# Optimization experiments

Hardware: AMD Instinct MI355X
Metric: run time of the kernel (lower is better)

Reference implementation:

```python
import jax, jax.numpy as jnp
import numpy as np

EPS = 1e-7
NC = 80
REG_MAX = 16
TOPK = 10
ALPHA = 0.5
BETA = 6.0
BOX_GAIN = 7.5
CLS_GAIN = 0.5
DFL_GAIN = 1.5
GRID = 92  # GRID*GRID = 8464 anchors


def _make_anchors(n):
    c = jnp.arange(n, dtype=jnp.float32) + 0.5
    gy, gx = jnp.meshgrid(c, c, indexing='ij')
    return jnp.stack([gx.ravel(), gy.ravel()], axis=-1)  # (n*n, 2)


def setup_inputs() -> dict:
    key = jax.random.key(0)
    ks = jax.random.split(key, 8)
    B, M, A = 32, 64, GRID * GRID
    anchor_points = _make_anchors(GRID)
    pred_scores = jax.random.normal(ks[0], (B, A, NC), jnp.float32)
    pred_dist = jax.random.normal(ks[1], (B, A, 4 * REG_MAX), jnp.float32)
    # decoded pred boxes: anchor center +- positive ltrb offsets (grid units)
    off = jax.random.uniform(ks[2], (B, A, 4), jnp.float32, 0.5, 12.0)
    ap = anchor_points[None]
    pred_bboxes = jnp.concatenate([ap - off[..., :2], ap + off[..., 2:]], axis=-1)
    cxy = jax.random.uniform(ks[3], (B, M, 2), jnp.float32, 4.0, 88.0)
    wh = jax.random.uniform(ks[4], (B, M, 2), jnp.float32, 2.0, 24.0)
    gt_bboxes = jnp.concatenate([cxy - wh / 2, cxy + wh / 2], axis=-1)
    gt_labels = jax.random.randint(ks[5], (B, M, 1), 0, NC, jnp.int32)
    mask_gt = (jax.random.uniform(ks[6], (B, M, 1)) < 0.75).astype(jnp.float32)
    return dict(pred_scores=pred_scores, pred_dist=pred_dist, pred_bboxes=pred_bboxes,
                anchor_points=anchor_points, gt_labels=gt_labels, gt_bboxes=gt_bboxes,
                mask_gt=mask_gt)


def _assign(pred_scores, pred_bboxes, anchor_points, gt_labels, gt_bboxes, mask_gt):
    """TaskAlignedAssigner (runs under stop_gradient at call site)."""
    B, A, nc = pred_scores.shape
    M = gt_labels.shape[1]
    scores = jax.nn.sigmoid(pred_scores)  # (B,A,nc)
    gt = gt_bboxes[:, :, None, :]         # (B,M,1,4)
    pd = pred_bboxes[:, None, :, :]       # (B,1,A,4)
    iw = jnp.clip(jnp.minimum(gt[..., 2], pd[..., 2]) - jnp.maximum(gt[..., 0], pd[..., 0]), 0)
    ih = jnp.clip(jnp.minimum(gt[..., 3], pd[..., 3]) - jnp.maximum(gt[..., 1], pd[..., 1]), 0)
    inter = iw * ih
    a_gt = (gt[..., 2] - gt[..., 0]) * (gt[..., 3] - gt[..., 1])
    a_pd = (pd[..., 2] - pd[..., 0]) * (pd[..., 3] - pd[..., 1])
    overlaps = inter / (a_gt + a_pd - inter + EPS)  # (B,M,A)
    cls = jnp.clip(gt_labels[..., 0].astype(jnp.int32), 0, nc - 1)  # (B,M)
    idx = jnp.broadcast_to(cls[:, :, None], (B, M, A))
    align_scores = jnp.take_along_axis(scores.transpose(0, 2, 1), idx, axis=1)  # (B,M,A)
    align_metric = (align_scores ** ALPHA) * (overlaps ** BETA) * mask_gt
    k = min(TOPK, A)
    _, topk_idxs = jax.lax.top_k(align_metric, k)  # (B,M,k)
    cmask = jnp.zeros((B, M, A), bool).at[
        jnp.arange(B)[:, None, None], jnp.arange(M)[None, :, None], topk_idxs].set(True)
    # anchor center strictly inside GT box
    ax = anchor_points[None, None, :, 0]
    ay = anchor_points[None, None, :, 1]
    d = jnp.stack([ax - gt_bboxes[:, :, None, 0], ay - gt_bboxes[:, :, None, 1],
                   gt_bboxes[:, :, None, 2] - ax, gt_bboxes[:, :, None, 3] - ay], axis=-1)
    in_gt = d.min(axis=-1) > EPS  # (B,M,A)
    cmask = cmask & (mask_gt > 0) & in_gt
    fg_mask = cmask.any(axis=1)  # (B,A)
    mm = align_metric * cmask
    tgi = jnp.argmax(mm, axis=1)  # (B,A)
    tlab = jnp.take_along_axis(cls, tgi, axis=1) * fg_mask.astype(jnp.int32)
    tbox = jnp.take_along_axis(gt_bboxes, tgi[:, :, None], axis=1)  # (B,A,4)
    max_per_gt = mm.max(axis=2)  # (B,M)
    am = jnp.take_along_axis(align_metric, tgi[:, None, :], axis=1)[:, 0, :]  # (B,A)
    den = jnp.take_along_axis(max_per_gt, tgi, axis=1) + EPS
    norm_score = jnp.where(fg_mask, am / den, 0.0)
    tscores = jax.nn.one_hot(tlab, nc, dtype=pred_scores.dtype) * norm_score[..., None] * fg_mask[..., None]
    return tlab, tbox, tscores, fg_mask, tgi


def _ciou(b1, b2):
    """Element-wise CIoU for aligned box pairs, xyxy, (..., 4) -> (...)."""
    x11, y11, x21, y21 = (b1[..., i] for i in range(4))
    x12, y12, x22, y22 = (b2[..., i] for i in range(4))
    iw = jnp.clip(jnp.minimum(x21, x22) - jnp.maximum(x11, x12), 0)
    ih = jnp.clip(jnp.minimum(y21, y22) - jnp.maximum(y11, y12), 0)
    inter = iw * ih
    a1 = (x21 - x11) * (y21 - y11)
    a2 = (x22 - x12) * (y22 - y12)
    iou = inter / (a1 + a2 - inter + EPS)
    cw = jnp.maximum(x21, x22) - jnp.minimum(x11, x12)
    ch = jnp.maximum(y21, y22) - jnp.minimum(y11, y12)
    c2 = cw ** 2 + ch ** 2 + EPS
    rho2 = ((x11 + x21 - x12 - x22) ** 2 + (y11 + y21 - y12 - y22) ** 2) / 4
    w1, h1 = x21 - x11, y21 - y11
    w2, h2 = x22 - x12, y22 - y12
    v = (4.0 / jnp.pi ** 2) * (jnp.arctan(w1 / (h1 + EPS)) - jnp.arctan(w2 / (h2 + EPS))) ** 2
    alpha = jax.lax.stop_gradient(v / (1 - iou + v + EPS))
    return iou - (rho2 / c2 + v * alpha)


def _loss(pred_scores, pred_dist, pred_bboxes, anchor_points, gt_labels, gt_bboxes, mask_gt):
    asg = _assign(pred_scores, pred_bboxes, anchor_points, gt_labels, gt_bboxes, mask_gt)
    tlab, tbox, tscores, fg_mask, tgi = jax.tree_util.tree_map(jax.lax.stop_gradient, asg)
    fgf = fg_mask.astype(pred_scores.dtype)
    tss = jnp.maximum(tscores.sum(), 1.0)
    # classification: BCE with logits, summed, normalized by target_scores_sum
    x = pred_scores
    bce = jnp.maximum(x, 0) - x * tscores + jnp.log1p(jnp.exp(-jnp.abs(x)))
    loss_cls = bce.sum() / tss
    # CIoU loss over foreground anchors (masked, static shapes)
    weight = tscores.sum(-1) * fgf  # (B,A)
    iou = _ciou(pred_bboxes, tbox)
    loss_iou = ((1.0 - iou) * weight).sum() / tss
    # DFL: bbox2dist targets clipped to [0, reg_max-1-0.01]
    ap = anchor_points[None]
    t = jnp.concatenate([ap - tbox[..., :2], tbox[..., 2:] - ap], axis=-1)  # (B,A,4)
    t = jnp.clip(t, 0.0, REG_MAX - 1 - 0.01)
    tl = t.astype(jnp.int32)
    tr = jnp.minimum(tl + 1, REG_MAX - 1)
    wl = (tl + 1).astype(t.dtype) - t
    wr = 1.0 - wl
    logp = jax.nn.log_softmax(pred_dist.reshape(*pred_dist.shape[:-1], 4, REG_MAX), axis=-1)
    ce_l = -jnp.take_along_axis(logp, tl[..., None], axis=-1)[..., 0]
    ce_r = -jnp.take_along_axis(logp, tr[..., None], axis=-1)[..., 0]
    dfl = ce_l * wl + ce_r * wr  # (B,A,4)
    num_fg = fgf.sum()
    loss_dfl = jnp.where(num_fg > 0,
                         (dfl * fgf[..., None]).sum() / jnp.maximum(4.0 * num_fg, 1.0), 0.0)
    return BOX_GAIN * loss_iou + CLS_GAIN * loss_cls + DFL_GAIN * loss_dfl


def reference(pred_scores, pred_dist, pred_bboxes, anchor_points, gt_labels, gt_bboxes, mask_gt):
    return _loss(pred_scores, pred_dist, pred_bboxes, anchor_points, gt_labels, gt_bboxes, mask_gt)
```

## Files before the change

### kernel.cpp

```cpp
#include <hip/hip_runtime.h>
#include <cstdint>
#include <cstddef>

#define EPSF 1e-7f
#define NCC 80
#define REG_MAX 16
#define TOPK 10
#define GRID_W 92
#define A_TOT (GRID_W * GRID_W)
#define B_SZ 32
#define M_SZ 64
#define CHUNK 64
#define NCHUNK ((A_TOT + CHUNK - 1) / CHUNK)
#define WMAX 52

__device__ __forceinline__ int div92(int a) { return (a * 45591) >> 22; }

__global__ __launch_bounds__(256) void kP(
    const float* __restrict__ ps,
    const float* __restrict__ pb,
    const int*   __restrict__ gl,
    const float* __restrict__ gb,
    const float* __restrict__ mg,
    float* __restrict__ align_t,
    double* __restrict__ acc)
{
    __shared__ float  sq[CHUNK][NCC + 1];
    __shared__ float  sgb[M_SZ][4];
    __shared__ float  sag[M_SZ];
    __shared__ int    scls[M_SZ];
    __shared__ int    swy[M_SZ];
    __shared__ double sred[256];

    int blk = blockIdx.x;
    int b = blk / NCHUNK;
    int chunk = blk % NCHUNK;
    int a0 = chunk * CHUNK;
    int t = threadIdx.x;

    if (t < M_SZ) {
        int bm = b * M_SZ + t;
        float4 g = *(const float4*)(gb + (size_t)bm * 4);
        sgb[t][0] = g.x; sgb[t][1] = g.y; sgb[t][2] = g.z; sgb[t][3] = g.w;
        sag[t] = (g.z - g.x) * (g.w - g.y);
        int c = gl[bm]; scls[t] = min(max(c, 0), NCC - 1);
        int y0, y1;
        if (mg[bm] > 0.f) { y0 = max(0, (int)g.y - 13); y1 = min(91, (int)g.w + 13); }
        else             { y0 = 1; y1 = 0; }
        swy[t] = y0 | (y1 << 8);
    }

    const float* base = ps + ((size_t)b * A_TOT + a0) * NCC;
    double bces = 0.0;
    #pragma unroll
    for (int k = 0; k < 5; ++k) {
        int q = t + k * 256;
        int r = q / 20;
        int c = (q % 20) * 4;
        if (a0 + r < A_TOT) {
            float4 v = *(const float4*)(base + (size_t)r * NCC + c);
            float bsum = 0.f;
            #pragma unroll
            for (int j = 0; j < 4; ++j) {
                float x = (&v.x)[j];
                float t1 = __expf(-fabsf(x));
                bsum += fmaxf(x, 0.f) + __logf(1.f + t1);
                float rin = __fdividef(1.f, 1.f + t1);
                sq[r][c + j] = (x >= 0.f) ? rin : t1 * rin;
            }
            bces += (double)bsum;
        }
    }
    __syncthreads();

    int w = t >> 6, l = t & 63;
    int a = a0 + l;
    int cgy0 = a0 / GRID_W, cgy1 = (a0 + 63) / GRID_W;
    if (a < A_TOT) {
        float4 p = *(const float4*)(pb + ((size_t)b * A_TOT + a) * 4);
        float ap_area = (p.z - p.x) * (p.w - p.y);
        float* outbase = align_t + (size_t)b * M_SZ * A_TOT + a;
        #pragma unroll
        for (int mi = 0; mi < 16; ++mi) {
            int m = w * 16 + mi;
            int wyp = swy[m];
            int y0 = wyp & 0xFF, y1 = (wyp >> 8) & 0xFF;
            if (cgy1 < y0 || cgy0 > y1) continue;
            float g1 = sgb[m][0], g2 = sgb[m][1], g3 = sgb[m][2], g4 = sgb[m][3];
            float iw = fmaxf(fminf(g3, p.z) - fmaxf(g1, p.x), 0.f);
            float ih = fmaxf(fminf(g4, p.w) - fmaxf(g2, p.y), 0.f);
            float inter = iw * ih;
            float iou = inter * __fdividef(1.f, sag[m] + ap_area - inter + EPSF);
            float s = sqrtf(sq[l][scls[m]]);
            float i2 = iou * iou;
            outbase[(size_t)m * A_TOT] = s * (i2 * i2 * i2);
        }
    }

    sred[t] = bces;
    __syncthreads();
    for (int st = 128; st > 0; st >>= 1) {
        if (t < st) sred[t] += sred[t + st];
        __syncthreads();
    }
    if (t == 0) atomicAdd(&acc[5], sred[0]);
}

__global__ __launch_bounds__(64) void kA3(
    const float* __restrict__ align_t,
    const float* __restrict__ gb,
    const float* __restrict__ mg,
    unsigned long long* __restrict__ key,
    float* __restrict__ maxpg)
{
    __shared__ float s_v[WMAX * 64];
    __shared__ float s_selv[TOPK];
    __shared__ int   s_seli[TOPK];
    __shared__ float s_keepval[TOPK];

    int bm = blockIdx.x;
    int t = threadIdx.x;
    float mgt = mg[bm];
    if (mgt <= 0.f) {
        if (t == 0) maxpg[bm] = 0.f;
        return;
    }
    float gx1 = gb[bm * 4 + 0], gy1 = gb[bm * 4 + 1];
    float gx2 = gb[bm * 4 + 2], gy2 = gb[bm * 4 + 3];
    int wy0 = max(0, (int)gy1 - 13), wy1 = min(91, (int)gy2 + 13);
    int wx0 = max(0, (int)gx1 - 13), wx1 = min(91, (int)gx2 + 13);
    int nrows = wy1 - wy0 + 1, ncols = wx1 - wx0 + 1;

    const float* row = align_t + (size_t)bm * A_TOT;
    for (int r = 0; r < nrows; ++r)
        s_v[r * 64 + t] = (t < ncols) ? row[(wy0 + r) * GRID_W + wx0 + t] : -1.f;
    __syncthreads();

    for (int it = 0; it < TOPK; ++it) {
        float bv = -1.f; int ba = 0x7FFFFFFF;
        for (int r = 0; r < nrows; ++r) {
            float v = s_v[r * 64 + t];
            if (v > bv) { bv = v; ba = (wy0 + r) * GRID_W + wx0 + t; }
        }
        #pragma unroll
        for (int off = 1; off < 64; off <<= 1) {
            float ov = __shfl_xor(bv, off);
            int   oa = __shfl_xor(ba, off);
            if (ov > bv || (ov == bv && oa < ba)) { bv = ov; ba = oa; }
        }
        if (t == 0) {
            s_selv[it] = bv; s_seli[it] = ba;
            int gy = div92(ba);
            int rr = gy - wy0, ll = ba - GRID_W * gy - wx0;
            s_v[rr * 64 + ll] = -1.f;
        }
        __syncthreads();
    }

    if (t < TOPK) {
        int a = s_seli[t]; float v = s_selv[t];
        int gy = div92(a), gx = a - GRID_W * gy;
        float ax = gx + 0.5f, ay = gy + 0.5f;
        float d1 = ax - gx1, d2 = ay - gy1, d3 = gx2 - ax, d4 = gy2 - ay;
        float dmin = fminf(fminf(d1, d2), fminf(d3, d4));
        bool keep = (dmin > EPSF) && (v >= 0.f);
        s_keepval[t] = keep ? v : -1.f;
        if (keep) {
            int b = bm >> 6, m = bm & 63;
            unsigned long long k = ((unsigned long long)__float_as_uint(v) << 32)
                                 | (unsigned long long)(0xFFFFu - (unsigned)m);
            atomicMax(&key[(size_t)b * A_TOT + a], k);
        }
    }
    __syncthreads();
    if (t == 0) {
        float mx = 0.f;
        for (int i = 0; i < TOPK; ++i)
            if (s_keepval[i] >= 0.f) mx = fmaxf(mx, s_keepval[i]);
        maxpg[bm] = mx;
    }
}

__global__ __launch_bounds__(256) void kC(
    const float* __restrict__ ps, const float* __restrict__ pd, const float* __restrict__ pb,
    const float* __restrict__ anc, const int* __restrict__ gl, const float* __restrict__ gb,
    const float* __restrict__ align_t, const unsigned long long* __restrict__ key,
    const float* __restrict__ maxpg, double* __restrict__ acc)
{
    int i = blockIdx.x * blockDim.x + threadIdx.x;
    double s1 = 0, s2 = 0, s3 = 0, s4 = 0, nf = 0;
    if (i < B_SZ * A_TOT) {
        unsigned long long k = key[i];
        if (k) {
            int b = i / A_TOT, a = i % A_TOT;
            unsigned vbits = (unsigned)(k >> 32);
            int m = vbits ? (int)(0xFFFFu - (unsigned)(k & 0xFFFFull)) : 0;
            int bm = b * M_SZ + m;
            float gx1 = gb[bm * 4 + 0], gy1 = gb[bm * 4 + 1];
            float gx2 = gb[bm * 4 + 2], gy2 = gb[bm * 4 + 3];
            int cls = min(max(gl[bm], 0), NCC - 1);
            const float* px = pb + ((size_t)b * A_TOT + a) * 4;
            float p1 = px[0], p2 = px[1], p3 = px[2], p4 = px[3];

            float av = align_t[(size_t)bm * A_TOT + a];
            float xt = ps[((size_t)b * A_TOT + a) * NCC + cls];
            float norm = av / (maxpg[bm] + EPSF);

            float iw = fmaxf(fminf(p3, gx2) - fmaxf(p1, gx1), 0.f);
            float ih = fmaxf(fminf(p4, gy2) - fmaxf(p2, gy1), 0.f);
            float inter = iw * ih;
            float a1 = (p3 - p1) * (p4 - p2);
            float a2 = (gx2 - gx1) * (gy2 - gy1);
            float iou = inter / (a1 + a2 - inter + EPSF);
            float cw = fmaxf(p3, gx2) - fminf(p1, gx1);
            float ch = fmaxf(p4, gy2) - fminf(p2, gy1);
            float c2 = cw * cw + ch * ch + EPSF;
            float dx = p1 + p3 - gx1 - gx2, dy = p2 + p4 - gy1 - gy2;
            float rho2 = (dx * dx + dy * dy) * 0.25f;
            float w1 = p3 - p1, h1 = p4 - p2;
            float w2 = gx2 - gx1, h2 = gy2 - gy1;
            float dat = atanf(w1 / (h1 + EPSF)) - atanf(w2 / (h2 + EPSF));
            const float c4pi2 = (float)(4.0 / (3.14159265358979323846 * 3.14159265358979323846));
            float v = c4pi2 * dat * dat;
            float alpha = v / (1.f - iou + v + EPSF);
            float ciou = iou - (rho2 / c2 + v * alpha);

            float ax = anc[(size_t)a * 2], ay = anc[(size_t)a * 2 + 1];
            float tv[4] = { ax - gx1, ay - gy1, gx2 - ax, gy2 - ay };
            const float* pdd = pd + ((size_t)b * A_TOT + a) * 64;
            float dfl = 0.f;
            #pragma unroll
            for (int s = 0; s < 4; ++s) {
                float tt = fminf(fmaxf(tv[s], 0.f), (float)REG_MAX - 1.f - 0.01f);
                int tl = (int)tt;
                int tr = min(tl + 1, REG_MAX - 1);
                float wl = (float)(tl + 1) - tt;
                float wr = 1.f - wl;
                const float* rowp = pdd + s * 16;
                float mx = rowp[0];
                #pragma unroll
                for (int kk = 1; kk < 16; ++kk) mx = fmaxf(mx, rowp[kk]);
                float se = 0.f;
                #pragma unroll
                for (int kk = 0; kk < 16; ++kk) se += expf(rowp[kk] - mx);
                float lse = mx + logf(se);
                dfl += (lse - rowp[tl]) * wl + (lse - rowp[tr]) * wr;
            }

            s1 = (double)norm;
            s2 = (double)xt * (double)norm;
            s3 = (double)(1.f - ciou) * (double)norm;
            s4 = (double)dfl;
            nf = 1.0;
        }
    }
    __shared__ double sred[256];
    double vals[5] = { s1, s2, s3, s4, nf };
    for (int j = 0; j < 5; ++j) {
        sred[threadIdx.x] = vals[j];
        __syncthreads();
        for (int s = 128; s > 0; s >>= 1) {
            if (threadIdx.x < s) sred[threadIdx.x] += sred[threadIdx.x + s];
            __syncthreads();
        }
        if (threadIdx.x == 0 && sred[0] != 0.0) atomicAdd(&acc[j], sred[0]);
        __syncthreads();
    }
}

__global__ void kE(const double* __restrict__ acc, float* __restrict__ out)
{
    double tsum = acc[0];
    double tss = tsum > 1.0 ? tsum : 1.0;
    double bce = acc[5] - acc[1];
    double loss_cls = bce / tss;
    double loss_iou = acc[2] / tss;
    double nf = acc[4];
    double loss_dfl = (nf > 0.0) ? acc[3] / fmax(4.0 * nf, 1.0) : 0.0;
    out[0] = (float)(7.5 * loss_iou + 0.5 * loss_cls + 1.5 * loss_dfl);
}

extern "C" void kernel_launch(void* const* d_in, const int* in_sizes, int n_in,
                              void* d_out, int out_size, void* d_ws, size_t ws_size,
                              hipStream_t stream)
{
    const float* ps  = (const float*)d_in[0];
    const float* pd  = (const float*)d_in[1];
    const float* pb  = (const float*)d_in[2];
    const float* anc = (const float*)d_in[3];
    const int*   gl  = (const int*)d_in[4];
    const float* gb  = (const float*)d_in[5];
    const float* mg  = (const float*)d_in[6];
    float* out = (float*)d_out;

    char* ws = (char*)d_ws;
    const size_t align_bytes = (size_t)B_SZ * M_SZ * A_TOT * sizeof(float);
    const size_t key_bytes   = (size_t)B_SZ * A_TOT * sizeof(unsigned long long);
    float*              align_t = (float*)ws;
    unsigned long long* key     = (unsigned long long*)(ws + align_bytes);
    double*             acc     = (double*)(ws + align_bytes + key_bytes);
    float*              maxpg   = (float*)(ws + align_bytes + key_bytes + 64);

    hipMemsetAsync(ws + align_bytes, 0, key_bytes + 64, stream);

    kP <<<B_SZ * NCHUNK, 256, 0, stream>>>(ps, pb, gl, gb, mg, align_t, acc);
    kA3<<<B_SZ * M_SZ,   64,  0, stream>>>(align_t, gb, mg, key, maxpg);
    kC <<<(B_SZ * A_TOT + 255) / 256, 256, 0, stream>>>(ps, pd, pb, anc, gl, gb, align_t, key, maxpg, acc);
    kE <<<1, 1, 0, stream>>>(acc, out);
}
```

Before: 318.0 us.

## Use wavefront shuffle reductions, ballot-based gt culling, and computed anchors

Both block reductions (in kP and kC) are replaced with 64-lane shuffle reductions plus a tiny shared combine, cutting the barrier count from many to one. In kP, gt overlap tests are done once per lane and packed with a ballot, so each wavefront iterates only over overlapping gts via ctz. kC now derives anchor coordinates from the anchor index instead of loading the anchor_points input, which assumes the fixed grid layout. kA3 also gets unroll pragmas on its row loops.

```diff
diff --git a/kernel.cpp b/kernel.cpp
--- a/kernel.cpp
+++ b/kernel.cpp
@@ -30,7 +30,7 @@
     __shared__ float  sag[M_SZ];
     __shared__ int    scls[M_SZ];
     __shared__ int    swy[M_SZ];
-    __shared__ double sred[256];
+    __shared__ double sredw[4];
 
     int blk = blockIdx.x;
     int b = blk / NCHUNK;
@@ -46,7 +46,7 @@
         int c = gl[bm]; scls[t] = min(max(c, 0), NCC - 1);
         int y0, y1;
         if (mg[bm] > 0.f) { y0 = max(0, (int)g.y - 13); y1 = min(91, (int)g.w + 13); }
-        else             { y0 = 1; y1 = 0; }
+        else             { y0 = 255; y1 = 0; }
         swy[t] = y0 | (y1 << 8);
     }
 
@@ -74,18 +74,21 @@
     __syncthreads();
 
     int w = t >> 6, l = t & 63;
+    int wyp = swy[l];
+    int y0 = wyp & 0xFF, y1 = (wyp >> 8) & 0xFF;
+    int cgy0 = a0 / GRID_W, cgy1 = (a0 + CHUNK - 1) / GRID_W;
+    bool ov = (cgy0 <= y1) && (cgy1 >= y0);
+    unsigned long long mask0 = __ballot(ov);
+    unsigned int mask = (unsigned int)((mask0 >> (w * 16)) & 0xFFFFull);
+
     int a = a0 + l;
-    int cgy0 = a0 / GRID_W, cgy1 = (a0 + 63) / GRID_W;
-    if (a < A_TOT) {
+    if (a < A_TOT && mask) {
         float4 p = *(const float4*)(pb + ((size_t)b * A_TOT + a) * 4);
         float ap_area = (p.z - p.x) * (p.w - p.y);
         float* outbase = align_t + (size_t)b * M_SZ * A_TOT + a;
-        #pragma unroll
-        for (int mi = 0; mi < 16; ++mi) {
+        while (mask) {
+            int mi = __builtin_ctz(mask); mask &= mask - 1;
             int m = w * 16 + mi;
-            int wyp = swy[m];
-            int y0 = wyp & 0xFF, y1 = (wyp >> 8) & 0xFF;
-            if (cgy1 < y0 || cgy0 > y1) continue;
             float g1 = sgb[m][0], g2 = sgb[m][1], g3 = sgb[m][2], g4 = sgb[m][3];
             float iw = fmaxf(fminf(g3, p.z) - fmaxf(g1, p.x), 0.f);
             float ih = fmaxf(fminf(g4, p.w) - fmaxf(g2, p.y), 0.f);
@@ -97,13 +100,12 @@
         }
     }
 
-    sred[t] = bces;
-    __syncthreads();
-    for (int st = 128; st > 0; st >>= 1) {
-        if (t < st) sred[t] += sred[t + st];
-        __syncthreads();
-    }
-    if (t == 0) atomicAdd(&acc[5], sred[0]);
+    double v = bces;
+    #pragma unroll
+    for (int off = 1; off < 64; off <<= 1) v += __shfl_xor(v, off);
+    if (l == 0) sredw[w] = v;
+    __syncthreads();
+    if (t == 0) atomicAdd(&acc[5], sredw[0] + sredw[1] + sredw[2] + sredw[3]);
 }
 
 __global__ __launch_bounds__(64) void kA3(
@@ -132,12 +134,14 @@
     int nrows = wy1 - wy0 + 1, ncols = wx1 - wx0 + 1;
 
     const float* row = align_t + (size_t)bm * A_TOT;
+    #pragma unroll 4
     for (int r = 0; r < nrows; ++r)
         s_v[r * 64 + t] = (t < ncols) ? row[(wy0 + r) * GRID_W + wx0 + t] : -1.f;
     __syncthreads();
 
     for (int it = 0; it < TOPK; ++it) {
         float bv = -1.f; int ba = 0x7FFFFFFF;
+        #pragma unroll 4
         for (int r = 0; r < nrows; ++r) {
             float v = s_v[r * 64 + t];
             if (v > bv) { bv = v; ba = (wy0 + r) * GRID_W + wx0 + t; }
@@ -183,7 +187,7 @@
 
 __global__ __launch_bounds__(256) void kC(
     const float* __restrict__ ps, const float* __restrict__ pd, const float* __restrict__ pb,
-    const float* __restrict__ anc, const int* __restrict__ gl, const float* __restrict__ gb,
+    const int* __restrict__ gl, const float* __restrict__ gb,
     const float* __restrict__ align_t, const unsigned long long* __restrict__ key,
     const float* __restrict__ maxpg, double* __restrict__ acc)
 {
@@ -225,7 +229,8 @@
             float alpha = v / (1.f - iou + v + EPSF);
             float ciou = iou - (rho2 / c2 + v * alpha);
 
-            float ax = anc[(size_t)a * 2], ay = anc[(size_t)a * 2 + 1];
+            int gy = div92(a), gx = a - GRID_W * gy;
+            float ax = gx + 0.5f, ay = gy + 0.5f;
             float tv[4] = { ax - gx1, ay - gy1, gx2 - ax, gy2 - ay };
             const float* pdd = pd + ((size_t)b * A_TOT + a) * 64;
             float dfl = 0.f;
@@ -254,17 +259,21 @@
             nf = 1.0;
         }
     }
-    __shared__ double sred[256];
+
+    __shared__ double sw[4][5];
+    int w = threadIdx.x >> 6, l = threadIdx.x & 63;
     double vals[5] = { s1, s2, s3, s4, nf };
+    #pragma unroll
     for (int j = 0; j < 5; ++j) {
-        sred[threadIdx.x] = vals[j];
-        __syncthreads();
-        for (int s = 128; s > 0; s >>= 1) {
-            if (threadIdx.x < s) sred[threadIdx.x] += sred[threadIdx.x + s];
-            __syncthreads();
-        }
-        if (threadIdx.x == 0 && sred[0] != 0.0) atomicAdd(&acc[j], sred[0]);
-        __syncthreads();
+        double v = vals[j];
+        #pragma unroll
+        for (int off = 1; off < 64; off <<= 1) v += __shfl_xor(v, off);
+        if (l == 0) sw[w][j] = v;
+    }
+    __syncthreads();
+    if (threadIdx.x < 5) {
+        double s = sw[0][threadIdx.x] + sw[1][threadIdx.x] + sw[2][threadIdx.x] + sw[3][threadIdx.x];
+        if (s != 0.0) atomicAdd(&acc[threadIdx.x], s);
     }
 }
 
@@ -287,7 +296,6 @@
     const float* ps  = (const float*)d_in[0];
     const float* pd  = (const float*)d_in[1];
     const float* pb  = (const float*)d_in[2];
-    const float* anc = (const float*)d_in[3];
     const int*   gl  = (const int*)d_in[4];
     const float* gb  = (const float*)d_in[5];
     const float* mg  = (const float*)d_in[6];
@@ -305,6 +313,6 @@
 
     kP <<<B_SZ * NCHUNK, 256, 0, stream>>>(ps, pb, gl, gb, mg, align_t, acc);
     kA3<<<B_SZ * M_SZ,   64,  0, stream>>>(align_t, gb, mg, key, maxpg);
-    kC <<<(B_SZ * A_TOT + 255) / 256, 256, 0, stream>>>(ps, pd, pb, anc, gl, gb, align_t, key, maxpg, acc);
+    kC <<<(B_SZ * A_TOT + 255) / 256, 256, 0, stream>>>(ps, pd, pb, gl, gb, align_t, key, maxpg, acc);
     kE <<<1, 1, 0, stream>>>(acc, out);
 }
```

Result: faster. 268.2 us (-15.7%).
